# Kernel optimization log

Hardware: AMD Instinct MI355X
Metric: run time of the kernel (lower is better)

## Reference

```python
import jax, jax.numpy as jnp
import numpy as np

# ---- fixed constants from stft2hcfp.__init__ ----
FS = 16000.0; FR = 2.0; FC = 27.5; TC = 1.0 / 4487.0; NPO = 48
N = int(FS / FR)                      # 8000 FFT length
HALF_N = int(round(N / 2))            # 4000
SQRT_N = float(np.sqrt(N))
HIGH_FREQ_IDX = int(round(1.0 / TC / FR) + 1)   # 2245
HIGH_QUEF_IDX = int(round(FS / FC)) + 1         # 583
CUT_Q = int(round(FS * TC))           # 4  (cepstrum cutoff)
TOTAL_BINS = 4 * 88                   # 352 log-freq bins
NUM_HARMONIC = 5

def _central_freqs():
    stop = 1.0 / TC
    nest = int(np.ceil(np.log2(stop / FC)) * NPO)
    cf = []
    for i in range(nest):
        c = FC * 2.0 ** (float(i) / NPO)
        if c < stop:
            cf.append(c)
        else:
            break
    return cf

CF = _central_freqs()   # 353 central frequencies
NEST = len(CF)

def _freq_matrix():
    # triangular log-frequency filterbank over linear freq axis
    f = (FS * np.linspace(0, 0.5, HALF_N, endpoint=True))[:HIGH_FREQ_IDX]
    W = np.zeros((NEST - 1, len(f)), np.float32)
    for i in range(1, NEST - 1):
        l = int(round(CF[i - 1] / FR)); r = int(round(CF[i + 1] / FR) + 1)
        if l >= r - 1:
            W[i, l] = 1.0
        else:
            for j in range(l, r):
                if CF[i - 1] < f[j] < CF[i]:
                    W[i, j] = (f[j] - CF[i - 1]) / (CF[i] - CF[i - 1])
                elif CF[i] < f[j] < CF[i + 1]:
                    W[i, j] = (CF[i + 1] - f[j]) / (CF[i + 1] - CF[i])
    return W

def _quef_matrix():
    q = np.arange(HIGH_QUEF_IDX) / FS + 1e-6
    fq = 1.0 / q
    W = np.zeros((NEST - 1, len(fq)), np.float32)
    for i in range(1, NEST - 1):
        for j in range(int(round(FS / CF[i + 1])), int(round(FS / CF[i - 1]) + 1)):
            if j >= len(fq):
                continue
            if CF[i - 1] < fq[j] < CF[i]:
                W[i, j] = (fq[j] - CF[i - 1]) / (CF[i] - CF[i - 1])
            elif CF[i] < fq[j] < CF[i + 1]:
                W[i, j] = (CF[i + 1] - fq[j]) / (CF[i + 1] - CF[i])
    return W

# harmonic shift indices: closest central freq to (k+1)*27.5 Hz, k=0..5
HIDS = [int(np.argmin(np.abs(np.asarray(CF) - (k + 1) * FC))) for k in range(NUM_HARMONIC + 1)]


def _nonlinear(x, g, cutoff):
    # relu + pow(g), then zero first/last `cutoff` rows along axis 1.
    # safe pow: grad is 0 where x<=0 (matches relu-masked torch behavior, no inf at 0)
    y = jnp.where(x > 0, jnp.where(x > 0, x, 1.0) ** g, 0.0)
    y = y.at[:, :cutoff].set(0.0).at[:, -cutoff:].set(0.0)
    return y


def setup_inputs() -> dict:
    key = jax.random.key(0)
    dx = jax.random.uniform(key, (8, 512, N), dtype=jnp.float32)  # [B, T, 8000] spectrogram
    return {
        "dx": dx,
        "W_freq": jnp.asarray(_freq_matrix()),   # [352, 2245]
        "W_quef": jnp.asarray(_quef_matrix()),   # [352, 583]
    }


def reference(dx, W_freq, W_quef):
    tfr0 = jnp.swapaxes(dx, 1, 2)                       # [B, F=8000, T]
    # CFP layer 1: real part of FFT over freq axis -> cepstrum, nonlinear g=0.6
    ceps = jnp.fft.fft(tfr0, axis=1).real / SQRT_N      # [B, 8000, T]
    ceps = _nonlinear(ceps, 0.6, CUT_Q)
    # log-frequency mappings (banded triangular filterbanks)
    tfr0h = tfr0[:, :HIGH_FREQ_IDX]                      # [B, 2245, T]
    cepsh = ceps[:, :HIGH_QUEF_IDX]                      # [B, 583, T]
    tfrL0 = jnp.einsum('kf,bft->bkt', W_freq, tfr0h)     # [B, 352, T]
    tfrLQ = jnp.einsum('kq,bqt->bkt', W_quef, cepsh)     # [B, 352, T]
    # harmonic stacking: shift down (spectral) / shift up (cepstral)
    har_s = [jnp.pad(tfrL0[:, h:TOTAL_BINS], ((0, 0), (0, h), (0, 0))) for h in HIDS]
    har_c = [jnp.pad(tfrLQ[:, :TOTAL_BINS - h], ((0, 0), (h, 0), (0, 0))) for h in HIDS]
    piece = jnp.concatenate([jnp.stack(har_s, axis=1), jnp.stack(har_c, axis=1)], axis=1)
    return jnp.swapaxes(piece, 2, 3)                     # [B, 12, T, 352]
```

## Files before the change

kernel.cpp:

```cpp
#include <hip/hip_runtime.h>
#include <hip/hip_bf16.h>
#include <limits.h>

typedef __attribute__((ext_vector_type(8))) short short8;
typedef __attribute__((ext_vector_type(4))) short short4v;
typedef __attribute__((ext_vector_type(4))) float f32x4;
typedef __attribute__((ext_vector_type(16))) float f32x16;

#define NN 8000
#define NCOL 4096
#define KBINS 352
#define QPAD 640
#define QH 320
#define BN 256
#define KC 8
#define NTILE 125
#define CUTQ 4
#define T_ 512
#define WFB 64
#define WQB 20

#define GLL16(g, l) __builtin_amdgcn_global_load_lds( \
    (const __attribute__((address_space(1))) unsigned int*)(g), \
    (__attribute__((address_space(3))) unsigned int*)(l), 16, 0, 0)

static __device__ __forceinline__ ushort bfc(float f){
  __hip_bfloat16 h = __float2bfloat16(f);
  return *reinterpret_cast<ushort*>(&h);
}
static __device__ __forceinline__ float b2f(ushort u){
  unsigned v = ((unsigned)u) << 16; float f; __builtin_memcpy(&f, &v, 4); return f;
}

__global__ void gen_cos_k(ushort* __restrict__ cosg, int HQI){
  int n = blockIdx.x*256 + threadIdx.x;
  int q = blockIdx.y;
  if (n >= NN) return;
  float v = 0.f;
  if (q < HQI){
    int m = (q*n) % NN;
    v = cosf((float)m * 7.8539816339744831e-4f);
  }
  int kt = n >> 6, s8 = (n >> 3) & 7, e = n & 7;
  cosg[(size_t)kt*(QPAD*64) + (size_t)q*64 + (((s8 ^ (q & 7)) << 3) | e)] = bfc(v);
}

__global__ void bounds_k(const float* __restrict__ W, int width,
                         int* __restrict__ lo, int* __restrict__ hi){
  __shared__ int slo, shi;
  int r = blockIdx.x;
  if (threadIdx.x==0){ slo = INT_MAX; shi = -1; }
  __syncthreads();
  int mylo = INT_MAX, myhi = -1;
  for (int c = threadIdx.x; c < width; c += 256){
    if (W[(size_t)r*width + c] != 0.f){ if (c < mylo) mylo = c; if (c > myhi) myhi = c; }
  }
  atomicMin(&slo, mylo); atomicMax(&shi, myhi);
  __syncthreads();
  if (threadIdx.x==0){
    if (shi < 0){ lo[r] = 0; hi[r] = 0; }
    else        { lo[r] = slo; hi[r] = shi + 1; }
  }
}

__global__ void pack_k(const float* __restrict__ W, const int* __restrict__ lo,
                       const int* __restrict__ hi, int width, int bw,
                       float* __restrict__ WT){
  int r = blockIdx.x;
  int l = lo[r], h = hi[r];
  for (int j = threadIdx.x; j < bw; j += 64){
    float v = 0.f;
    if (l + j < h) v = W[(size_t)r*width + l + j];
    WT[(size_t)j*KBINS + r] = v;
  }
}

__global__ __launch_bounds__(512, 2) void gemm_k(const float* __restrict__ dx,
                                                 const ushort* __restrict__ cosg,
                                                 ushort* __restrict__ part){
  __shared__ ushort As[2][QH*64];
  __shared__ ushort Bs[2][BN*64];
  int tid = threadIdx.x;
  int nb = blockIdx.x, qh = blockIdx.y, kc = blockIdx.z;
  int lane = tid & 63, widx = tid >> 6;
  int wm = widx & 1, wn = widx >> 1;
  int l31 = lane & 31, lh = lane >> 5;
  int kt0 = kc*16, ktE = (kc < 7) ? kt0 + 16 : NTILE;

  int srow = widx*4 + (lane >> 4);
  int sfo  = (lane & 15) * 4;
  int slot16 = (lane & 15) >> 1, shalf = (lane & 15) & 1;
  const ushort* cg0 = cosg + (size_t)qh*(QH*64);

  f32x16 acc[5][2];
  #pragma unroll
  for (int a=0;a<5;a++){ acc[a][0] = (f32x16)0.f; acc[a][1] = (f32x16)0.f; }

  f32x4 d[8];
  #define DX_LOAD(kt_) { _Pragma("unroll") \
    for (int i=0;i<8;i++){ int row = i*32 + srow; \
      d[i] = *(const f32x4*)(dx + (size_t)(nb*BN + row)*NN + (size_t)(kt_)*64 + sfo); } }
  #define DX_WRITE(buf) { _Pragma("unroll") \
    for (int i=0;i<8;i++){ int row = i*32 + srow; \
      short4v s; s[0]=(short)bfc(d[i][0]); s[1]=(short)bfc(d[i][1]); \
                 s[2]=(short)bfc(d[i][2]); s[3]=(short)bfc(d[i][3]); \
      *(short4v*)(&Bs[buf][row*64 + (((slot16 ^ (row & 7)) << 3) | (shalf << 2))]) = s; } }
  #define COS_STAGE(kt_, buf) { const ushort* cg = cg0 + (size_t)(kt_)*(QPAD*64) + tid*8; \
    _Pragma("unroll") \
    for (int i=0;i<5;i++) GLL16(cg + i*4096, &As[buf][i*4096 + tid*8]); }

  DX_LOAD(kt0);
  COS_STAGE(kt0, 0);
  DX_WRITE(0);
  __syncthreads();

  int cur = 0;
  for (int kt = kt0; kt < ktE; ++kt){
    if (kt + 1 < ktE){
      COS_STAGE(kt+1, cur^1);
      DX_LOAD(kt+1);
    }
    const ushort* Ac = &As[cur][0];
    const ushort* Bc = &Bs[cur][0];
    #pragma unroll
    for (int p=0;p<4;p++){
      short8 dfr[2];
      #pragma unroll
      for (int c=0;c<2;c++){
        int row = wn*64 + c*32 + l31;
        dfr[c] = *(const short8*)(Bc + row*64 + ((((p<<1)|lh) ^ (row & 7)) << 3));
      }
      short8 cfr[5];
      #pragma unroll
      for (int a=0;a<5;a++){
        int row = wm*160 + a*32 + l31;
        cfr[a] = *(const short8*)(Ac + row*64 + ((((p<<1)|lh) ^ (row & 7)) << 3));
      }
      #pragma unroll
      for (int a=0;a<5;a++){
        acc[a][0] = __builtin_amdgcn_mfma_f32_32x32x16_bf16(dfr[0], cfr[a], acc[a][0], 0,0,0);
        acc[a][1] = __builtin_amdgcn_mfma_f32_32x32x16_bf16(dfr[1], cfr[a], acc[a][1], 0,0,0);
      }
    }
    if (kt + 1 < ktE) DX_WRITE(cur^1);
    __syncthreads();
    cur ^= 1;
  }

  ushort* pb = part + (size_t)kc*NCOL*QPAD;
  #pragma unroll
  for (int a=0;a<5;a++){
    int q = qh*QH + wm*160 + a*32 + l31;
    #pragma unroll
    for (int c=0;c<2;c++){
      int colb = nb*BN + wn*64 + c*32 + 4*lh;
      #pragma unroll
      for (int r=0;r<16;r++){
        int col = colb + (r&3) + 8*(r>>2);
        pb[(size_t)col*QPAD + q] = bfc(acc[a][c][r]);
      }
    }
  }
}

__global__ __launch_bounds__(384) void fuse_k(const float* __restrict__ dx,
        const ushort* __restrict__ part,
        const float* __restrict__ WfT, const float* __restrict__ WqT,
        const int* __restrict__ fLo, const int* __restrict__ qLo,
        float* __restrict__ out, int HFI, int HQI){
  __shared__ float xr[2368];
  __shared__ float yq[QPAD];
  __shared__ float tl0[KBINS];
  __shared__ float tlq[KBINS];
  int col = blockIdx.x;
  int b = col >> 9, t = col & 511;
  int tid = threadIdx.x;
  const float invs = 0.011180339887498949f;

  for (int f = tid; f < 2368; f += 384) xr[f] = (f < HFI) ? dx[(size_t)col*NN + f] : 0.f;
  const ushort* pc = part + (size_t)col*QPAD;
  for (int q = tid; q < QPAD; q += 384){
    float y = 0.f;
    if (q < HQI){
      float s = 0.f;
      #pragma unroll
      for (int kc=0; kc<KC; kc++) s += b2f(pc[(size_t)kc*NCOL*QPAD + q]);
      s *= invs;
      if (q >= CUTQ && s > 0.f) y = powf(s, 0.6f);
    }
    yq[q] = y;
  }
  __syncthreads();

  if (tid < KBINS){
    int k = tid;
    int lo = fLo[k];
    float aF = 0.f;
    #pragma unroll
    for (int j=0;j<WFB;j++) aF += WfT[j*KBINS + k] * xr[lo + j];
    int ql = qLo[k];
    float aQ = 0.f;
    #pragma unroll
    for (int j=0;j<WQB;j++) aQ += WqT[j*KBINS + k] * yq[ql + j];
    tl0[k] = aF; tlq[k] = aQ;
  }
  __syncthreads();

  const int hids[6] = {0,48,76,96,111,124};
  for (int u = tid; u < 12*KBINS; u += 384){
    int j = u / KBINS;
    int k = u - j*KBINS;
    int h = hids[(j < 6) ? j : j - 6];
    float v;
    if (j < 6) v = (k + h < KBINS) ? tl0[k + h] : 0.f;
    else       v = (k >= h)        ? tlq[k - h] : 0.f;
    out[(((size_t)b*12 + j)*T_ + t)*KBINS + k] = v;
  }
}

extern "C" void kernel_launch(void* const* d_in, const int* in_sizes, int n_in,
                              void* d_out, int out_size, void* d_ws, size_t ws_size,
                              hipStream_t stream){
  const float* dx = (const float*)d_in[0];
  const float* Wf = (const float*)d_in[1];
  const float* Wq = (const float*)d_in[2];
  int HFI = in_sizes[1] / KBINS;
  int HQI = in_sizes[2] / KBINS;
  float* out = (float*)d_out;
  char* ws = (char*)d_ws;

  ushort* cosg = (ushort*)ws;
  size_t off = (size_t)NTILE*QPAD*64*2;
  ushort* part = (ushort*)(ws + off); off += (size_t)KC*NCOL*QPAD*2;
  int* fLo = (int*)(ws+off); off += KBINS*4;
  int* fHi = (int*)(ws+off); off += KBINS*4;
  int* qLo = (int*)(ws+off); off += KBINS*4;
  int* qHi = (int*)(ws+off); off += KBINS*4;
  float* WfT = (float*)(ws+off); off += (size_t)WFB*KBINS*4;
  float* WqT = (float*)(ws+off); off += (size_t)WQB*KBINS*4;
  (void)n_in; (void)out_size; (void)ws_size;

  gen_cos_k<<<dim3((NN+255)/256, QPAD), 256, 0, stream>>>(cosg, HQI);
  bounds_k<<<KBINS, 256, 0, stream>>>(Wf, HFI, fLo, fHi);
  bounds_k<<<KBINS, 256, 0, stream>>>(Wq, HQI, qLo, qHi);
  pack_k<<<KBINS, 64, 0, stream>>>(Wf, fLo, fHi, HFI, WFB, WfT);
  pack_k<<<KBINS, 64, 0, stream>>>(Wq, qLo, qHi, HQI, WQB, WqT);
  gemm_k<<<dim3(NCOL/BN, QPAD/QH, KC), 512, 0, stream>>>(dx, cosg, part);
  fuse_k<<<NCOL, 384, 0, stream>>>(dx, part, WfT, WqT, fLo, qLo, out, HFI, HQI);
}
```

Baseline: 139.7 us.

## Fold DFT cosine symmetry to halve GEMM reduction length

Uses the even symmetry of the cosine DFT kernel, cos(2πqn/N) = cos(2πq(N-n)/N), to pre-add x[n] and x[N-n] while staging the input. This halves the reduction dimension from 8000 to about 4000 (63 tiles). The cosine table generation is shrunk to match, and K-splits drop from 8 to 7. Staging is now split into two halves interleaved with the MFMA compute, and s_setprio is raised around the MFMA blocks. The cost is extra global loads of the mirrored addresses plus per-element adds and branches during staging.

```diff
diff --git a/kernel.cpp b/kernel.cpp
--- a/kernel.cpp
+++ b/kernel.cpp
@@ -3,7 +3,6 @@
 #include <limits.h>
 
 typedef __attribute__((ext_vector_type(8))) short short8;
-typedef __attribute__((ext_vector_type(4))) short short4v;
 typedef __attribute__((ext_vector_type(4))) float f32x4;
 typedef __attribute__((ext_vector_type(16))) float f32x16;
 
@@ -13,8 +12,9 @@
 #define QPAD 640
 #define QH 320
 #define BN 256
-#define KC 8
-#define NTILE 125
+#define KC 7
+#define NTILE 63
+#define KSTEP 9
 #define CUTQ 4
 #define T_ 512
 #define WFB 64
@@ -35,7 +35,7 @@
 __global__ void gen_cos_k(ushort* __restrict__ cosg, int HQI){
   int n = blockIdx.x*256 + threadIdx.x;
   int q = blockIdx.y;
-  if (n >= NN) return;
+  if (n >= NTILE*64) return;
   float v = 0.f;
   if (q < HQI){
     int m = (q*n) % NN;
@@ -74,6 +74,8 @@
     WT[(size_t)j*KBINS + r] = v;
   }
 }
+
+struct SR { f32x4 p0, p1, ma, mb; float ms; };
 
 __global__ __launch_bounds__(512, 2) void gemm_k(const float* __restrict__ dx,
                                                  const ushort* __restrict__ cosg,
@@ -85,64 +87,79 @@
   int lane = tid & 63, widx = tid >> 6;
   int wm = widx & 1, wn = widx >> 1;
   int l31 = lane & 31, lh = lane >> 5;
-  int kt0 = kc*16, ktE = (kc < 7) ? kt0 + 16 : NTILE;
-
-  int srow = widx*4 + (lane >> 4);
-  int sfo  = (lane & 15) * 4;
-  int slot16 = (lane & 15) >> 1, shalf = (lane & 15) & 1;
-  const ushort* cg0 = cosg + (size_t)qh*(QH*64);
+  int kt0 = kc*KSTEP, ktE = kt0 + KSTEP;
+
+  int srow = tid >> 3;
+  int sfo  = (tid & 7) * 8;
+
+  #define LOADS(s_, kt_, pass_) { \
+    int row_ = (pass_)*64 + srow; \
+    const float* rp_ = dx + (size_t)(nb*BN + row_)*NN; \
+    int n0_ = (kt_)*64 + sfo; \
+    s_.p0 = *(const f32x4*)(rp_ + n0_); \
+    s_.p1 = *(const f32x4*)(rp_ + n0_ + 4); \
+    s_.ma = *(const f32x4*)(rp_ + 7996 - n0_); \
+    s_.mb = *(const f32x4*)(rp_ + 7992 - n0_); \
+    s_.ms = rp_[n0_ ? NN - n0_ : 0]; }
+
+  #define WRITES(s_, kt_, pass_, buf_) { \
+    int row_ = (pass_)*64 + srow; \
+    int n0_ = (kt_)*64 + sfo; \
+    float pr_[8] = {s_.p0[0],s_.p0[1],s_.p0[2],s_.p0[3],s_.p1[0],s_.p1[1],s_.p1[2],s_.p1[3]}; \
+    float mi_[8] = {n0_ ? s_.ms : 0.f, s_.ma[3],s_.ma[2],s_.ma[1],s_.ma[0], s_.mb[3],s_.mb[2],s_.mb[1]}; \
+    short8 o_; \
+    _Pragma("unroll") \
+    for (int e_=0;e_<8;e_++){ \
+      int n_ = n0_ + e_; \
+      float v_ = (n_ < 4000) ? pr_[e_] + mi_[e_] : ((n_ == 4000) ? pr_[e_] : 0.f); \
+      o_[e_] = (short)bfc(v_); } \
+    *(short8*)(&Bs[buf_][row_*64 + (((tid & 7) ^ (row_ & 7)) << 3)]) = o_; }
+
+  #define COSG(kt_, buf_) { \
+    const ushort* cg_ = cosg + (size_t)(kt_)*(QPAD*64) + (size_t)qh*(QH*64) + tid*8; \
+    _Pragma("unroll") \
+    for (int i_=0;i_<5;i_++) GLL16(cg_ + i_*4096, &As[buf_][i_*4096 + tid*8]); }
 
   f32x16 acc[5][2];
   #pragma unroll
   for (int a=0;a<5;a++){ acc[a][0] = (f32x16)0.f; acc[a][1] = (f32x16)0.f; }
 
-  f32x4 d[8];
-  #define DX_LOAD(kt_) { _Pragma("unroll") \
-    for (int i=0;i<8;i++){ int row = i*32 + srow; \
-      d[i] = *(const f32x4*)(dx + (size_t)(nb*BN + row)*NN + (size_t)(kt_)*64 + sfo); } }
-  #define DX_WRITE(buf) { _Pragma("unroll") \
-    for (int i=0;i<8;i++){ int row = i*32 + srow; \
-      short4v s; s[0]=(short)bfc(d[i][0]); s[1]=(short)bfc(d[i][1]); \
-                 s[2]=(short)bfc(d[i][2]); s[3]=(short)bfc(d[i][3]); \
-      *(short4v*)(&Bs[buf][row*64 + (((slot16 ^ (row & 7)) << 3) | (shalf << 2))]) = s; } }
-  #define COS_STAGE(kt_, buf) { const ushort* cg = cg0 + (size_t)(kt_)*(QPAD*64) + tid*8; \
+  #define COMPUTE_HALF(h_, buf_) { \
+    const ushort* Ac_ = &As[buf_][0]; const ushort* Bc_ = &Bs[buf_][0]; \
     _Pragma("unroll") \
-    for (int i=0;i<5;i++) GLL16(cg + i*4096, &As[buf][i*4096 + tid*8]); }
-
-  DX_LOAD(kt0);
-  COS_STAGE(kt0, 0);
-  DX_WRITE(0);
+    for (int p_=2*(h_); p_<2*(h_)+2; p_++){ \
+      short8 dfr_[2]; \
+      _Pragma("unroll") \
+      for (int c_=0;c_<2;c_++){ int row_ = wn*64 + c_*32 + l31; \
+        dfr_[c_] = *(const short8*)(Bc_ + row_*64 + ((((p_<<1)|lh) ^ (row_ & 7)) << 3)); } \
+      short8 cfr_[5]; \
+      _Pragma("unroll") \
+      for (int a_=0;a_<5;a_++){ int row_ = wm*160 + a_*32 + l31; \
+        cfr_[a_] = *(const short8*)(Ac_ + row_*64 + ((((p_<<1)|lh) ^ (row_ & 7)) << 3)); } \
+      __builtin_amdgcn_s_setprio(1); \
+      _Pragma("unroll") \
+      for (int a_=0;a_<5;a_++){ \
+        acc[a_][0] = __builtin_amdgcn_mfma_f32_32x32x16_bf16(dfr_[0], cfr_[a_], acc[a_][0], 0,0,0); \
+        acc[a_][1] = __builtin_amdgcn_mfma_f32_32x32x16_bf16(dfr_[1], cfr_[a_], acc[a_][1], 0,0,0); } \
+      __builtin_amdgcn_s_setprio(0); } }
+
+  SR s0, s1;
+  LOADS(s0, kt0, 0); LOADS(s1, kt0, 1);
+  COSG(kt0, 0);
+  WRITES(s0, kt0, 0, 0); WRITES(s1, kt0, 1, 0);
+  LOADS(s0, kt0, 2); LOADS(s1, kt0, 3);
+  WRITES(s0, kt0, 2, 0); WRITES(s1, kt0, 3, 0);
   __syncthreads();
 
   int cur = 0;
   for (int kt = kt0; kt < ktE; ++kt){
-    if (kt + 1 < ktE){
-      COS_STAGE(kt+1, cur^1);
-      DX_LOAD(kt+1);
-    }
-    const ushort* Ac = &As[cur][0];
-    const ushort* Bc = &Bs[cur][0];
-    #pragma unroll
-    for (int p=0;p<4;p++){
-      short8 dfr[2];
-      #pragma unroll
-      for (int c=0;c<2;c++){
-        int row = wn*64 + c*32 + l31;
-        dfr[c] = *(const short8*)(Bc + row*64 + ((((p<<1)|lh) ^ (row & 7)) << 3));
-      }
-      short8 cfr[5];
-      #pragma unroll
-      for (int a=0;a<5;a++){
-        int row = wm*160 + a*32 + l31;
-        cfr[a] = *(const short8*)(Ac + row*64 + ((((p<<1)|lh) ^ (row & 7)) << 3));
-      }
-      #pragma unroll
-      for (int a=0;a<5;a++){
-        acc[a][0] = __builtin_amdgcn_mfma_f32_32x32x16_bf16(dfr[0], cfr[a], acc[a][0], 0,0,0);
-        acc[a][1] = __builtin_amdgcn_mfma_f32_32x32x16_bf16(dfr[1], cfr[a], acc[a][1], 0,0,0);
-      }
-    }
-    if (kt + 1 < ktE) DX_WRITE(cur^1);
+    bool stg = (kt + 1 < ktE);
+    if (stg){ COSG(kt+1, cur^1); LOADS(s0, kt+1, 0); LOADS(s1, kt+1, 1); }
+    COMPUTE_HALF(0, cur);
+    if (stg){ WRITES(s0, kt+1, 0, cur^1); WRITES(s1, kt+1, 1, cur^1);
+              LOADS(s0, kt+1, 2); LOADS(s1, kt+1, 3); }
+    COMPUTE_HALF(1, cur);
+    if (stg){ WRITES(s0, kt+1, 2, cur^1); WRITES(s1, kt+1, 3, cur^1); }
     __syncthreads();
     cur ^= 1;
   }
@@ -240,7 +257,7 @@
   float* WqT = (float*)(ws+off); off += (size_t)WQB*KBINS*4;
   (void)n_in; (void)out_size; (void)ws_size;
 
-  gen_cos_k<<<dim3((NN+255)/256, QPAD), 256, 0, stream>>>(cosg, HQI);
+  gen_cos_k<<<dim3((NTILE*64+255)/256, QPAD), 256, 0, stream>>>(cosg, HQI);
   bounds_k<<<KBINS, 256, 0, stream>>>(Wf, HFI, fLo, fHi);
   bounds_k<<<KBINS, 256, 0, stream>>>(Wq, HQI, qLo, qHi);
   pack_k<<<KBINS, 64, 0, stream>>>(Wf, fLo, fHi, HFI, WFB, WfT);
```

Result: faster. 133.6 us (-4.3%).

## Fold real input by cosine symmetry to halve DFT GEMM K dimension

Applied to the files above, without the earlier changes.

A new fold kernel uses the even symmetry of the cosine transform (x[n]+x[N-n]) to cut the reduction length from 8000 to about 4001. It writes the folded input as swizzled bf16 tiles, which lets the GEMM load both operands with direct global-to-LDS copies instead of converting fp32 in registers. The GEMM tiling changes to BN=128 with KC=4 splits and 16 k-steps each, and s_setprio is set around the MFMA block. This adds a separate pass that reads all of dx and a larger workspace buffer. The folded values are summed before rounding to bf16, which changes rounding behaviour.

```diff
diff --git a/kernel.cpp b/kernel.cpp
--- a/kernel.cpp
+++ b/kernel.cpp
@@ -3,7 +3,6 @@
 #include <limits.h>
 
 typedef __attribute__((ext_vector_type(8))) short short8;
-typedef __attribute__((ext_vector_type(4))) short short4v;
 typedef __attribute__((ext_vector_type(4))) float f32x4;
 typedef __attribute__((ext_vector_type(16))) float f32x16;
 
@@ -12,9 +11,10 @@
 #define KBINS 352
 #define QPAD 640
 #define QH 320
-#define BN 256
-#define KC 8
-#define NTILE 125
+#define BN 128
+#define KC 4
+#define NTILE 64
+#define KSTEP 16
 #define CUTQ 4
 #define T_ 512
 #define WFB 64
@@ -35,7 +35,6 @@
 __global__ void gen_cos_k(ushort* __restrict__ cosg, int HQI){
   int n = blockIdx.x*256 + threadIdx.x;
   int q = blockIdx.y;
-  if (n >= NN) return;
   float v = 0.f;
   if (q < HQI){
     int m = (q*n) % NN;
@@ -43,6 +42,30 @@
   }
   int kt = n >> 6, s8 = (n >> 3) & 7, e = n & 7;
   cosg[(size_t)kt*(QPAD*64) + (size_t)q*64 + (((s8 ^ (q & 7)) << 3) | e)] = bfc(v);
+}
+
+__global__ __launch_bounds__(512) void fold_k(const float* __restrict__ dx,
+                                              ushort* __restrict__ xf){
+  int row = blockIdx.x;
+  int tid = threadIdx.x;
+  const float* rp = dx + (size_t)row*NN;
+  int n0 = tid*8;
+  f32x4 p0 = *(const f32x4*)(rp + n0);
+  f32x4 p1 = *(const f32x4*)(rp + n0 + 4);
+  f32x4 ma = *(const f32x4*)(rp + 7996 - n0);
+  f32x4 mb = *(const f32x4*)(rp + 7992 - n0);
+  float ms = rp[n0 ? NN - n0 : 0];
+  float pr[8] = {p0[0],p0[1],p0[2],p0[3],p1[0],p1[1],p1[2],p1[3]};
+  float mi[8] = {n0 ? ms : 0.f, ma[3],ma[2],ma[1],ma[0],mb[3],mb[2],mb[1]};
+  short8 o;
+  #pragma unroll
+  for (int e=0;e<8;e++){
+    int n = n0 + e;
+    float v = (n < 4000) ? pr[e] + mi[e] : ((n == 4000) ? pr[e] : 0.f);
+    o[e] = (short)bfc(v);
+  }
+  int kt = n0 >> 6, s8 = (n0 >> 3) & 7;
+  *(short8*)(&xf[((size_t)kt*NCOL + row)*64 + ((s8 ^ (row & 7)) << 3)]) = o;
 }
 
 __global__ void bounds_k(const float* __restrict__ W, int width,
@@ -75,7 +98,7 @@
   }
 }
 
-__global__ __launch_bounds__(512, 2) void gemm_k(const float* __restrict__ dx,
+__global__ __launch_bounds__(512, 2) void gemm_k(const ushort* __restrict__ xf,
                                                  const ushort* __restrict__ cosg,
                                                  ushort* __restrict__ part){
   __shared__ ushort As[2][QH*64];
@@ -85,64 +108,47 @@
   int lane = tid & 63, widx = tid >> 6;
   int wm = widx & 1, wn = widx >> 1;
   int l31 = lane & 31, lh = lane >> 5;
-  int kt0 = kc*16, ktE = (kc < 7) ? kt0 + 16 : NTILE;
-
-  int srow = widx*4 + (lane >> 4);
-  int sfo  = (lane & 15) * 4;
-  int slot16 = (lane & 15) >> 1, shalf = (lane & 15) & 1;
-  const ushort* cg0 = cosg + (size_t)qh*(QH*64);
-
-  f32x16 acc[5][2];
+  int kt0 = kc*KSTEP, ktE = kt0 + KSTEP;
+
+  const ushort* ag0 = cosg + (size_t)qh*(QH*64) + tid*8;
+  const ushort* bg0 = xf + (size_t)nb*(BN*64) + tid*8;
+
+  #define STAGE(kt_, buf_) { \
+    const ushort* ag_ = ag0 + (size_t)(kt_)*(QPAD*64); \
+    _Pragma("unroll") \
+    for (int i_=0;i_<5;i_++) GLL16(ag_ + i_*4096, &As[buf_][tid*8 + i_*4096]); \
+    const ushort* bg_ = bg0 + (size_t)(kt_)*(NCOL*64); \
+    GLL16(bg_,        &Bs[buf_][tid*8]); \
+    GLL16(bg_ + 4096, &Bs[buf_][tid*8 + 4096]); }
+
+  f32x16 acc[5];
   #pragma unroll
-  for (int a=0;a<5;a++){ acc[a][0] = (f32x16)0.f; acc[a][1] = (f32x16)0.f; }
-
-  f32x4 d[8];
-  #define DX_LOAD(kt_) { _Pragma("unroll") \
-    for (int i=0;i<8;i++){ int row = i*32 + srow; \
-      d[i] = *(const f32x4*)(dx + (size_t)(nb*BN + row)*NN + (size_t)(kt_)*64 + sfo); } }
-  #define DX_WRITE(buf) { _Pragma("unroll") \
-    for (int i=0;i<8;i++){ int row = i*32 + srow; \
-      short4v s; s[0]=(short)bfc(d[i][0]); s[1]=(short)bfc(d[i][1]); \
-                 s[2]=(short)bfc(d[i][2]); s[3]=(short)bfc(d[i][3]); \
-      *(short4v*)(&Bs[buf][row*64 + (((slot16 ^ (row & 7)) << 3) | (shalf << 2))]) = s; } }
-  #define COS_STAGE(kt_, buf) { const ushort* cg = cg0 + (size_t)(kt_)*(QPAD*64) + tid*8; \
-    _Pragma("unroll") \
-    for (int i=0;i<5;i++) GLL16(cg + i*4096, &As[buf][i*4096 + tid*8]); }
-
-  DX_LOAD(kt0);
-  COS_STAGE(kt0, 0);
-  DX_WRITE(0);
+  for (int a=0;a<5;a++) acc[a] = (f32x16)0.f;
+
+  STAGE(kt0, 0);
   __syncthreads();
 
   int cur = 0;
   for (int kt = kt0; kt < ktE; ++kt){
-    if (kt + 1 < ktE){
-      COS_STAGE(kt+1, cur^1);
-      DX_LOAD(kt+1);
-    }
+    if (kt + 1 < ktE) STAGE(kt+1, cur^1);
     const ushort* Ac = &As[cur][0];
     const ushort* Bc = &Bs[cur][0];
     #pragma unroll
     for (int p=0;p<4;p++){
-      short8 dfr[2];
-      #pragma unroll
-      for (int c=0;c<2;c++){
-        int row = wn*64 + c*32 + l31;
-        dfr[c] = *(const short8*)(Bc + row*64 + ((((p<<1)|lh) ^ (row & 7)) << 3));
-      }
+      int brow = wn*32 + l31;
+      short8 dfr = *(const short8*)(Bc + brow*64 + ((((p<<1)|lh) ^ (brow & 7)) << 3));
       short8 cfr[5];
       #pragma unroll
       for (int a=0;a<5;a++){
-        int row = wm*160 + a*32 + l31;
-        cfr[a] = *(const short8*)(Ac + row*64 + ((((p<<1)|lh) ^ (row & 7)) << 3));
+        int arow = wm*160 + a*32 + l31;
+        cfr[a] = *(const short8*)(Ac + arow*64 + ((((p<<1)|lh) ^ (arow & 7)) << 3));
       }
+      __builtin_amdgcn_s_setprio(1);
       #pragma unroll
-      for (int a=0;a<5;a++){
-        acc[a][0] = __builtin_amdgcn_mfma_f32_32x32x16_bf16(dfr[0], cfr[a], acc[a][0], 0,0,0);
-        acc[a][1] = __builtin_amdgcn_mfma_f32_32x32x16_bf16(dfr[1], cfr[a], acc[a][1], 0,0,0);
-      }
+      for (int a=0;a<5;a++)
+        acc[a] = __builtin_amdgcn_mfma_f32_32x32x16_bf16(dfr, cfr[a], acc[a], 0,0,0);
+      __builtin_amdgcn_s_setprio(0);
     }
-    if (kt + 1 < ktE) DX_WRITE(cur^1);
     __syncthreads();
     cur ^= 1;
   }
@@ -151,14 +157,11 @@
   #pragma unroll
   for (int a=0;a<5;a++){
     int q = qh*QH + wm*160 + a*32 + l31;
-    #pragma unroll
-    for (int c=0;c<2;c++){
-      int colb = nb*BN + wn*64 + c*32 + 4*lh;
-      #pragma unroll
-      for (int r=0;r<16;r++){
-        int col = colb + (r&3) + 8*(r>>2);
-        pb[(size_t)col*QPAD + q] = bfc(acc[a][c][r]);
-      }
+    int colb = nb*BN + wn*32 + 4*lh;
+    #pragma unroll
+    for (int r=0;r<16;r++){
+      int col = colb + (r&3) + 8*(r>>2);
+      pb[(size_t)col*QPAD + q] = bfc(acc[a][r]);
     }
   }
 }
@@ -231,6 +234,7 @@
 
   ushort* cosg = (ushort*)ws;
   size_t off = (size_t)NTILE*QPAD*64*2;
+  ushort* xf = (ushort*)(ws + off); off += (size_t)NTILE*NCOL*64*2;
   ushort* part = (ushort*)(ws + off); off += (size_t)KC*NCOL*QPAD*2;
   int* fLo = (int*)(ws+off); off += KBINS*4;
   int* fHi = (int*)(ws+off); off += KBINS*4;
@@ -240,11 +244,12 @@
   float* WqT = (float*)(ws+off); off += (size_t)WQB*KBINS*4;
   (void)n_in; (void)out_size; (void)ws_size;
 
-  gen_cos_k<<<dim3((NN+255)/256, QPAD), 256, 0, stream>>>(cosg, HQI);
+  gen_cos_k<<<dim3(16, QPAD), 256, 0, stream>>>(cosg, HQI);
+  fold_k<<<NCOL, 512, 0, stream>>>(dx, xf);
   bounds_k<<<KBINS, 256, 0, stream>>>(Wf, HFI, fLo, fHi);
   bounds_k<<<KBINS, 256, 0, stream>>>(Wq, HQI, qLo, qHi);
   pack_k<<<KBINS, 64, 0, stream>>>(Wf, fLo, fHi, HFI, WFB, WfT);
   pack_k<<<KBINS, 64, 0, stream>>>(Wq, qLo, qHi, HQI, WQB, WqT);
-  gemm_k<<<dim3(NCOL/BN, QPAD/QH, KC), 512, 0, stream>>>(dx, cosg, part);
+  gemm_k<<<dim3(NCOL/BN, QPAD/QH, KC), 512, 0, stream>>>(xf, cosg, part);
   fuse_k<<<NCOL, 384, 0, stream>>>(dx, part, WfT, WqT, fLo, qLo, out, HFI, HQI);
 }
```

After: 141.6 us. Within noise of the previous version (+1.4%).
